# Kernel optimization log

Hardware: AMD Instinct MI355X
Metric: run time of the kernel (lower is better)

Reference implementation:

```python
import jax, jax.numpy as jnp
import numpy as np

N_FILTERS = 40
FILTER_SIZE = 401   # int(16000*25/1000), forced odd
POOL_STRIDE = 160   # int(16000*10/1000)
EPS = 1e-6
S_SMOOTH = 0.04     # fixed PCEN smoothing coefficient s
DELTA = 2.0         # fixed PCEN bias delta
R_MIN, R_MAX = 0.2, 1.0
HIDDEN = 32


def setup_inputs() -> dict:
    key = jax.random.key(0)
    ks = jax.random.split(key, 6)
    B, L = 8, 160000
    x = jax.random.normal(ks[0], (B, L), dtype=jnp.float32)
    # mel-initialized Gabor params (as in mel_filter_params)
    sr, fmin, fmax = 16000.0, 60.0, 7800.0
    min_mel = 1127.0 * np.log1p(fmin / 700.0)
    max_mel = 1127.0 * np.log1p(fmax / 700.0)
    peaks_mel = np.linspace(min_mel, max_mel, N_FILTERS + 2)
    peaks_hz = 700.0 * np.expm1(peaks_mel / 1127.0)
    center_freqs = jnp.asarray(peaks_hz[1:-1] * 2.0 * np.pi / sr, dtype=jnp.float32)
    z = np.sqrt(2.0 * np.log(2.0)) / np.pi
    bandwidths = jnp.asarray(z * sr / (peaks_hz[2:] - peaks_hz[:-2]), dtype=jnp.float32)
    pooling_widths = jnp.full((N_FILTERS,), 0.4, dtype=jnp.float32)
    # GRU (input_size=1, hidden=32) + head Linear(32,32)->ReLU->Linear(32,2)
    def gl(k, shape):
        return jax.random.normal(k, shape, dtype=jnp.float32) * 0.1
    w_ih = gl(ks[1], (3 * HIDDEN, 1))
    w_hh = gl(ks[2], (3 * HIDDEN, HIDDEN))
    b_ih = jnp.zeros((3 * HIDDEN,), jnp.float32)
    b_hh = jnp.zeros((3 * HIDDEN,), jnp.float32)
    hw1 = gl(ks[3], (32, HIDDEN)); hb1 = jnp.zeros((32,), jnp.float32)
    hw2 = gl(ks[4], (2, 32)); hb2 = jnp.zeros((2,), jnp.float32)
    return dict(x=x, center_freqs=center_freqs, bandwidths=bandwidths,
                pooling_widths=pooling_widths, w_ih=w_ih, w_hh=w_hh,
                b_ih=b_ih, b_hh=b_hh, hw1=hw1, hb1=hb1, hw2=hw2, hb2=hb2)


def _gabor_filterbank(x, center_freqs, bandwidths, pooling_widths):
    z = np.sqrt(2.0 * np.log(2.0)) / np.pi
    cf = jnp.clip(center_freqs, 0.0, np.pi)
    bw = jnp.clip(bandwidths, 4.0 * z, FILTER_SIZE * z)
    t = jnp.arange(-(FILTER_SIZE // 2), (FILTER_SIZE + 1) // 2, dtype=jnp.float32)
    denom = 1.0 / (jnp.sqrt(2.0 * np.pi) * bw)                        # [F]
    gauss = jnp.exp(-(t[None, :] ** 2) / (2.0 * bw[:, None] ** 2))    # [F,K]
    phase = cf[:, None] * t[None, :]                                  # [F,K]
    fr = denom[:, None] * gauss * jnp.cos(phase)
    fi = denom[:, None] * gauss * jnp.sin(phase)
    filt = jnp.concatenate([fr, fi], axis=0)[:, None, :]              # [2F,1,K]
    pad = FILTER_SIZE // 2
    y = jax.lax.conv_general_dilated(x[:, None, :], filt, (1,), [(pad, pad)])
    y = y ** 2
    y = y[:, :N_FILTERS] + y[:, N_FILTERS:]                           # squared modulus [B,F,L]
    pw = jnp.clip(pooling_widths, 2.0 / FILTER_SIZE, 0.5)
    tt = jnp.arange(FILTER_SIZE, dtype=jnp.float32) / (FILTER_SIZE - 1) - 0.5
    win = jnp.exp(-0.5 * (tt[None, :] / pw[:, None]) ** 2)[:, None, :]  # [F,1,K]
    y = jax.lax.conv_general_dilated(y, win, (POOL_STRIDE,), [(pad, pad)],
                                     feature_group_count=N_FILTERS)
    return y  # [B,F,T]


def _gru_cell(h, xin, w_ih, w_hh, b_ih, b_hh):
    gi = xin @ w_ih.T + b_ih   # [N,3H]
    gh = h @ w_hh.T + b_hh
    i_r, i_z, i_n = jnp.split(gi, 3, axis=-1)
    h_r, h_z, h_n = jnp.split(gh, 3, axis=-1)
    r = jax.nn.sigmoid(i_r + h_r)
    zz = jax.nn.sigmoid(i_z + h_z)
    n = jnp.tanh(i_n + r * h_n)
    return (1.0 - zz) * n + zz * h


def _adaptive_pcen(frames, w_ih, w_hh, b_ih, b_hh, hw1, hb1, hw2, hb2):
    B, F, T = frames.shape
    Xt = jnp.transpose(frames, (2, 0, 1))  # [T,B,F]

    def controller(x_prev, x_t):  # each [B,F] -> per-bin (alpha, r)
        xp = x_prev.reshape(-1, 1)
        xc = x_t.reshape(-1, 1)
        h = jnp.zeros((B * F, HIDDEN), frames.dtype)
        h = _gru_cell(h, xp, w_ih, w_hh, b_ih, b_hh)
        h = _gru_cell(h, xc, w_ih, w_hh, b_ih, b_hh)
        hid = jax.nn.relu(h @ hw1.T + hb1)
        logits = hid @ hw2.T + hb2  # [B*F,2]
        alpha = jax.nn.sigmoid(logits[:, 0]).reshape(B, F)
        r = (R_MIN + (R_MAX - R_MIN) * jax.nn.sigmoid(logits[:, 1])).reshape(B, F)
        return alpha, r

    def step(carry, X_t):
        M_prev, X_prev = carry
        alpha, r = controller(X_prev, X_t)
        M_t = (1.0 - S_SMOOTH) * M_prev + S_SMOOTH * X_t
        out = (X_t / (M_t + EPS) ** alpha + DELTA) ** r - DELTA ** r
        return (M_t, X_t), out

    init = (jnp.zeros((B, F), frames.dtype), Xt[0])
    _, outs = jax.lax.scan(step, init, Xt)
    return jnp.transpose(outs, (1, 2, 0))  # [B,F,T]


def reference(x, center_freqs, bandwidths, pooling_widths,
              w_ih, w_hh, b_ih, b_hh, hw1, hb1, hw2, hb2):
    frames = _gabor_filterbank(x, center_freqs, bandwidths, pooling_widths)
    return _adaptive_pcen(frames, w_ih, w_hh, b_ih, b_hh, hw1, hb1, hw2, hb2)
```

## Files before the change

### kernel.cpp

```cpp
#include <hip/hip_runtime.h>
#include <math.h>

#define NF 40
#define FS 401
#define AST 424
#define PSTRIDE 160
#define BB 8
#define LL 160000
#define PADL 256
#define LST 161024
#define TOUT 1000
#define NTILE 512
#define NCHUNKC 313
#define ROWCH 121
#define ROWST (ROWCH*8)
#define EROW 522
#define WLEN 416
#define NCONVB 5032

typedef __attribute__((ext_vector_type(8))) _Float16 half8v;
typedef __attribute__((ext_vector_type(4))) _Float16 half4v;
typedef __attribute__((ext_vector_type(2))) _Float16 half2v;
typedef __attribute__((ext_vector_type(4))) float float4v;
typedef _Float16 f16;

__device__ __forceinline__ float sigm(float x) { return 1.0f / (1.0f + __expf(-x)); }
__device__ __forceinline__ float tanh_fast(float x) { return 1.0f - 2.0f / (__expf(2.0f * x) + 1.0f); }

__global__ __launch_bounds__(256) void prep_all(
    const float* __restrict__ x, const float* __restrict__ cf_,
    const float* __restrict__ bw_, const float* __restrict__ pw_,
    f16* __restrict__ xb, f16* __restrict__ Ag, float* __restrict__ Wg)
{
    int blk = blockIdx.x;
    if (blk < NCONVB) {
        int i = blk * 256 + threadIdx.x;
        int b = i / LST, o = i % LST;
        float v = 0.0f;
        if (o >= PADL && o < PADL + LL) v = x[b * LL + (o - PADL)];
        xb[i] = (f16)v;
        return;
    }
    if (blk < NCONVB + 80) {
        const float PI_F = 3.14159265358979323846f;
        int row = blk - NCONVB;
        int f = row >> 1, comp = row & 1;
        float Z = sqrtf(2.0f * logf(2.0f)) / PI_F;
        float cf = fminf(fmaxf(cf_[f], 0.0f), PI_F);
        float bw = fminf(fmaxf(bw_[f], 4.0f * Z), 401.0f * Z);
        float denom = 1.0f / (sqrtf(2.0f * PI_F) * bw);
        float inv2 = 1.0f / (2.0f * bw * bw);
        for (int k = threadIdx.x; k < AST; k += 256) {
            float v = 0.0f;
            if (k < FS) {
                float t = (float)(k - 200);
                float g = denom * expf(-(t * t) * inv2);
                float sv, cv;
                sincosf(cf * t, &sv, &cv);
                v = comp ? g * sv : g * cv;
            }
            Ag[row * AST + k] = (f16)v;
        }
        return;
    }
    int f = blk - (NCONVB + 80);
    float pw = fminf(fmaxf(pw_[f], 2.0f / 401.0f), 0.5f);
    float invpw = 1.0f / pw;
    for (int k = threadIdx.x; k < WLEN; k += 256) {
        float w = 0.0f;
        if (k < FS) {
            float ttv = (float)k * (1.0f / 400.0f) - 0.5f;
            float u = ttv * invpw;
            w = expf(-0.5f * u * u);
        }
        Wg[f * WLEN + k] = w;
    }
}

__global__ __launch_bounds__(256, 2) void conv_pool(
    const f16* __restrict__ xb,
    const f16* __restrict__ Ag,
    const float* __restrict__ Wg,
    float* __restrict__ Pp)
{
    __shared__ __align__(16) unsigned char smem[40 * EROW * 2];
    f16* slab = (f16*)smem;
    f16* eL   = (f16*)smem;

    int chunk = blockIdx.x;
    int bi = blockIdx.y;
    int p0 = chunk * NTILE;
    int pbase = PADL + p0 - 200;
    const f16* xs = xb + (size_t)bi * LST;
    int tid = threadIdx.x;

    for (int sc = tid; sc < 8 * 120; sc += 256) {
        int r = sc / 120, m = sc - r * 120;
        int s0 = pbase + 8 * m + (r & ~1);
        const uint* gp = (const uint*)(xs + s0);
        uint v0 = gp[0], v1 = gp[1], v2 = gp[2], v3 = gp[3], v4 = gp[4];
        if (r & 1) {
            v0 = __builtin_amdgcn_alignbyte(v1, v0, 2);
            v1 = __builtin_amdgcn_alignbyte(v2, v1, 2);
            v2 = __builtin_amdgcn_alignbyte(v3, v2, 2);
            v3 = __builtin_amdgcn_alignbyte(v4, v3, 2);
        }
        *(uint4*)(&slab[r * ROWST + 8 * m]) = make_uint4(v0, v1, v2, v3);
    }
    __syncthreads();

    int wv = tid >> 6, lane = tid & 63, q = lane >> 4, l15 = lane & 15;

    float4v acc[5][8];
#pragma unroll
    for (int t = 0; t < 5; ++t)
#pragma unroll
        for (int s = 0; s < 8; ++s)
            acc[t][s] = (float4v){0.f, 0.f, 0.f, 0.f};

    const f16* aP[5];
    const f16* bPtr[10];
#pragma unroll
    for (int t = 0; t < 5; ++t) aP[t] = Ag + (16 * t + l15) * AST + 8 * q;
#pragma unroll
    for (int s = 0; s < 10; ++s) {
        int pos = 128 * wv + 16 * s + l15;
        bPtr[s] = slab + (pos & 7) * ROWST + 8 * ((pos >> 3) + q);
    }

    half8v bf[8];
#pragma unroll
    for (int s = 0; s < 8; ++s) bf[s] = *(const half8v*)(bPtr[s]);

#pragma unroll
    for (int kk = 0; kk < 13; ++kk) {
        int k = 32 * kk;
        half8v af[5];
#pragma unroll
        for (int t = 0; t < 5; ++t) af[t] = *(const half8v*)(aP[t] + k);
        half8v nb0, nb1;
        if (kk < 12) {
            nb0 = *(const half8v*)(bPtr[8] + k);
            nb1 = *(const half8v*)(bPtr[9] + k);
        }
#pragma unroll
        for (int t = 0; t < 5; ++t)
#pragma unroll
            for (int s = 0; s < 8; ++s)
                acc[t][s] = __builtin_amdgcn_mfma_f32_16x16x32_f16(af[t], bf[s], acc[t][s], 0, 0, 0);
        if (kk < 12) {
#pragma unroll
            for (int s = 0; s < 6; ++s) bf[s] = bf[s + 2];
            bf[6] = nb0; bf[7] = nb1;
        }
    }

    __syncthreads();

#pragma unroll
    for (int t = 0; t < 5; ++t) {
        int f0 = 8 * t + 2 * q;
#pragma unroll
        for (int s = 0; s < 8; ++s) {
            float4v a = acc[t][s];
            int pl = 128 * wv + 16 * s + l15;
            bool ok = (p0 + pl) < LL;
            eL[f0 * EROW + pl] = ok ? (f16)(a.x * a.x + a.y * a.y) : (f16)0.f;
            eL[(f0 + 1) * EROW + pl] = ok ? (f16)(a.z * a.z + a.w * a.w) : (f16)0.f;
        }
    }
    for (int i = tid; i < 40 * 10; i += 256) {
        int r = i / 10, cc = 512 + (i - r * 10);
        eL[r * EROW + cc] = (f16)0.f;
    }
    __syncthreads();

    int tau_lo = (p0 - 41) / 160;
    if (tau_lo < 0) tau_lo = 0;
    int tau_hi = (p0 + 711) / 160;
    if (tau_hi > TOUT - 1) tau_hi = TOUT - 1;
    int npr = (tau_hi - tau_lo + 1) * 40;
    int slot = chunk & 1;

    if (tid < npr) {
        int ta = tid / 40;
        int f = tid - ta * 40;
        int tau = tau_lo + ta;
        int base = tau * 160 - 200 - p0;
        int kstart = base < 0 ? -base : 0;
        int kend = 512 - base; if (kend > 401) kend = 401;
        const f16* ep = eL + f * EROW + base + kstart;
        const float* wp = Wg + f * WLEN + kstart;
        float pa = 0.0f;
#pragma unroll 4
        for (int k = kstart; k < kend; k += 2) {
            half2v e2 = *(const half2v*)ep;
            float2 w2 = *(const float2*)wp;
            pa = fmaf((float)e2[0], w2.x, pa);
            pa = fmaf((float)e2[1], w2.y, pa);
            ep += 2; wp += 2;
        }
        Pp[(((size_t)bi * NF + f) * TOUT + tau) * 2 + slot] = pa;
    }
}

__global__ __launch_bounds__(256) void pcen_scan_kernel(
    const float* __restrict__ Pp, float* __restrict__ X, float* __restrict__ M)
{
    int wid = (blockIdx.x * 256 + threadIdx.x) >> 6;
    int lane = threadIdx.x & 63;
    if (wid >= BB * NF) return;
    const float a1 = 0.96f;
    const float a2 = a1 * a1;
    const float a4 = a2 * a2;
    const float a8 = a4 * a4;
    const float a16 = a8 * a8;
    const float a32 = a16 * a16;
    const float ss = 0.04f;
    float al1 = powf(a1, (float)(lane + 1));
    float carry = 0.0f;
    const float* prow = Pp + (size_t)wid * TOUT * 2;
    float* xrow = X + (size_t)wid * TOUT;
    float* mrow = M + (size_t)wid * TOUT;

    for (int c = 0; c < TOUT; c += 64) {
        int t = c + lane;
        float v = 0.0f;
        if (t < TOUT) {
            int s = t * 160 - 200;
            int cl = (s > 0) ? (s >> 9) : 0;
            int ch = (s + 400) >> 9;
            if (ch > NCHUNKC - 1) ch = NCHUNKC - 1;
            v = prow[2 * t + (cl & 1)];
            if (ch > cl) v += prow[2 * t + ((cl & 1) ^ 1)];
            xrow[t] = v;
        }
        float y = ss * v;
        float u;
        u = __shfl_up(y, 1, 64);  if (lane >= 1)  y = fmaf(a1, u, y);
        u = __shfl_up(y, 2, 64);  if (lane >= 2)  y = fmaf(a2, u, y);
        u = __shfl_up(y, 4, 64);  if (lane >= 4)  y = fmaf(a4, u, y);
        u = __shfl_up(y, 8, 64);  if (lane >= 8)  y = fmaf(a8, u, y);
        u = __shfl_up(y, 16, 64); if (lane >= 16) y = fmaf(a16, u, y);
        u = __shfl_up(y, 32, 64); if (lane >= 32) y = fmaf(a32, u, y);
        y = fmaf(al1, carry, y);
        carry = __shfl(y, 63, 64);
        if (t < TOUT) mrow[t] = y;
    }
}

__global__ __launch_bounds__(256) void pcen_ctrl_mfma(
    const float* __restrict__ X, const float* __restrict__ M,
    const float* __restrict__ w_ih, const float* __restrict__ w_hh,
    const float* __restrict__ b_ih, const float* __restrict__ b_hh,
    const float* __restrict__ hw1, const float* __restrict__ hb1,
    const float* __restrict__ hw2, const float* __restrict__ hb2,
    float* __restrict__ out)
{
    __shared__ f16 s_whhA[96 * 40];
    __shared__ f16 s_w1A[32 * 40];
    __shared__ __align__(16) float4 s_A1[32];
    __shared__ __align__(16) float4 s_A2[32];
    __shared__ float s_hb1[32];
    __shared__ float s_hw2[64];
    __shared__ float s_hb2[2];
    __shared__ f16 sh1[4][16 * 40];
    __shared__ f16 sh2[4][16 * 40];
    __shared__ float sxc[4][16], sxp[4][16], smv[4][16];

    int tid = threadIdx.x;
    for (int i = tid; i < 96 * 32; i += 256) {
        int m = i >> 5, k = i & 31;
        s_whhA[m * 40 + k] = (f16)w_hh[i];
    }
    for (int i = tid; i < 32 * 32; i += 256) {
        int m = i >> 5, k = i & 31;
        s_w1A[m * 40 + k] = (f16)hw1[i];
    }
    if (tid < 32) {
        int j = tid;
        s_A1[j] = make_float4(w_ih[j], b_ih[j] + b_hh[j],
                              w_ih[32 + j], b_ih[32 + j] + b_hh[32 + j]);
        s_A2[j] = make_float4(w_ih[64 + j], b_ih[64 + j], b_hh[64 + j], 0.0f);
        s_hb1[j] = hb1[j];
    }
    if (tid < 64) s_hw2[tid] = hw2[tid];
    if (tid < 2)  s_hb2[tid] = hb2[tid];
    __syncthreads();

    int wv = tid >> 6, lane = tid & 63;
    int c = lane & 15, q = lane >> 4;
    int instBase = blockIdx.x * 64 + wv * 16;

    if (lane < 16) {
        int idx = instBase + lane;
        int t = idx % TOUT;
        float xcv = X[idx];
        float xpv = (t == 0) ? xcv : X[idx - 1];
        sxc[wv][lane] = xcv;
        sxp[wv][lane] = xpv;
        smv[wv][lane] = M[idx];
    }
    float xp = sxp[wv][c];
    float xc = sxc[wv][c];
    float mv = smv[wv][c];

    float h1v[8];
#pragma unroll
    for (int jj = 0; jj < 8; ++jj) {
        int j = (jj < 4) ? (4 * q + jj) : (16 + 4 * q + (jj - 4));
        float4 a1 = s_A1[j];
        float4 a2 = s_A2[j];
        float r = sigm(fmaf(xp, a1.x, a1.y));
        float z = sigm(fmaf(xp, a1.z, a1.w));
        float n = tanh_fast(fmaf(xp, a2.x, a2.y) + r * a2.z);
        h1v[jj] = (1.0f - z) * n;
    }

    {
        half4v lo = {(f16)h1v[0], (f16)h1v[1], (f16)h1v[2], (f16)h1v[3]};
        half4v hi = {(f16)h1v[4], (f16)h1v[5], (f16)h1v[6], (f16)h1v[7]};
        *(half4v*)(&sh1[wv][c * 40 + 4 * q]) = lo;
        *(half4v*)(&sh1[wv][c * 40 + 16 + 4 * q]) = hi;
    }

    float4v acc[6];
    {
        half8v bf = *(const half8v*)(&sh1[wv][c * 40 + 8 * q]);
#pragma unroll
        for (int t = 0; t < 6; ++t) {
            half8v af = *(const half8v*)(&s_whhA[(16 * t + c) * 40 + 8 * q]);
            acc[t] = __builtin_amdgcn_mfma_f32_16x16x32_f16(af, bf, (float4v){0.f,0.f,0.f,0.f}, 0, 0, 0);
        }
    }

    float h2v[8];
#pragma unroll
    for (int jj = 0; jj < 8; ++jj) {
        int j = (jj < 4) ? (4 * q + jj) : (16 + 4 * q + (jj - 4));
        int reg = jj & 3;
        float accR = (jj < 4) ? acc[0][reg] : acc[1][reg];
        float accZ = (jj < 4) ? acc[2][reg] : acc[3][reg];
        float accN = (jj < 4) ? acc[4][reg] : acc[5][reg];
        float4 a1 = s_A1[j];
        float4 a2 = s_A2[j];
        float r = sigm(fmaf(xc, a1.x, a1.y) + accR);
        float z = sigm(fmaf(xc, a1.z, a1.w) + accZ);
        float gn = accN + a2.z;
        float n = tanh_fast(fmaf(xc, a2.x, a2.y) + r * gn);
        h2v[jj] = fmaf(z, h1v[jj] - n, n);
    }

    {
        half4v lo = {(f16)h2v[0], (f16)h2v[1], (f16)h2v[2], (f16)h2v[3]};
        half4v hi = {(f16)h2v[4], (f16)h2v[5], (f16)h2v[6], (f16)h2v[7]};
        *(half4v*)(&sh2[wv][c * 40 + 4 * q]) = lo;
        *(half4v*)(&sh2[wv][c * 40 + 16 + 4 * q]) = hi;
    }

    float4v hacc[2];
    {
        half8v bf = *(const half8v*)(&sh2[wv][c * 40 + 8 * q]);
#pragma unroll
        for (int t = 0; t < 2; ++t) {
            half8v af = *(const half8v*)(&s_w1A[(16 * t + c) * 40 + 8 * q]);
            hacc[t] = __builtin_amdgcn_mfma_f32_16x16x32_f16(af, bf, (float4v){0.f,0.f,0.f,0.f}, 0, 0, 0);
        }
    }

    float p0 = 0.f, p1 = 0.f;
#pragma unroll
    for (int jj = 0; jj < 8; ++jj) {
        int i = (jj < 4) ? (4 * q + jj) : (16 + 4 * q + (jj - 4));
        int reg = jj & 3;
        float hv = (jj < 4) ? hacc[0][reg] : hacc[1][reg];
        hv = fmaxf(hv + s_hb1[i], 0.0f);
        p0 = fmaf(hv, s_hw2[i], p0);
        p1 = fmaf(hv, s_hw2[32 + i], p1);
    }
    p0 += __shfl_xor(p0, 16);
    p0 += __shfl_xor(p0, 32);
    p1 += __shfl_xor(p1, 16);
    p1 += __shfl_xor(p1, 32);

    float alpha = sigm(p0 + s_hb2[0]);
    float rr = fmaf(0.8f, sigm(p1 + s_hb2[1]), 0.2f);
    float md = __expf(alpha * __logf(mv + 1e-6f));
    float bse = xc / md + 2.0f;
    float val = __expf(rr * __logf(bse)) - __expf(rr * 0.69314718056f);
    if (lane < 16)
        out[instBase + lane] = val;
}

extern "C" void kernel_launch(void* const* d_in, const int* in_sizes, int n_in,
                              void* d_out, int out_size, void* d_ws, size_t ws_size,
                              hipStream_t stream) {
    const float* x    = (const float*)d_in[0];
    const float* cf   = (const float*)d_in[1];
    const float* bw   = (const float*)d_in[2];
    const float* pw   = (const float*)d_in[3];
    const float* w_ih = (const float*)d_in[4];
    const float* w_hh = (const float*)d_in[5];
    const float* b_ih = (const float*)d_in[6];
    const float* b_hh = (const float*)d_in[7];
    const float* hw1  = (const float*)d_in[8];
    const float* hb1  = (const float*)d_in[9];
    const float* hw2  = (const float*)d_in[10];
    const float* hb2  = (const float*)d_in[11];
    float* out = (float*)d_out;

    f16* xb   = (f16*)d_ws;
    f16* Ag   = xb + (size_t)BB * LST;
    float* Wg = (float*)(Ag + (size_t)80 * AST);
    float* Pp = Wg + (size_t)NF * WLEN;
    float* Xf = Pp + (size_t)BB * NF * TOUT * 2;
    float* Mf = Xf + (size_t)BB * NF * TOUT;

    prep_all<<<dim3(NCONVB + 80 + 40), dim3(256), 0, stream>>>(
        x, cf, bw, pw, xb, Ag, Wg);

    conv_pool<<<dim3(NCHUNKC, BB), dim3(256), 0, stream>>>(xb, Ag, Wg, Pp);

    pcen_scan_kernel<<<dim3((BB * NF * 64) / 256), dim3(256), 0, stream>>>(Pp, Xf, Mf);
    pcen_ctrl_mfma<<<dim3((BB * NF * TOUT) / 64), dim3(256), 0, stream>>>(
        Xf, Mf, w_ih, w_hh, b_ih, b_hh, hw1, hb1, hw2, hb2, out);
}
```

Before: 296.0 us.

## Parallelize pooling dot products across 16-lane groups with fp16 shifted windows

The pooling stage in conv_pool used to give each (tau, filter) pair to one thread running a long serial loop. It now gives each pair to a 16-lane group that does 8-wide fp16 vector loads from four pre-shifted fp16 copies of the pooling window, then combines the partial sums with shuffles. This removes the serial tail and the misaligned fp32 window reads. In support, Pp is transposed to a tau-major layout, the conv_pool occupancy hint rises from 2 to 3 blocks, and the controller kernel handles four 64-instance groups per block. The trade-off is reduced precision from fp16 pooling weights and more shuffle work.

After: 583.1 us. 1.97x slower.

```diff
diff --git a/kernel.cpp b/kernel.cpp
--- a/kernel.cpp
+++ b/kernel.cpp
@@ -14,8 +14,8 @@
 #define NCHUNKC 313
 #define ROWCH 121
 #define ROWST (ROWCH*8)
-#define EROW 522
-#define WLEN 416
+#define EROW 520
+#define WL2 432
 #define NCONVB 5032
 
 typedef __attribute__((ext_vector_type(8))) _Float16 half8v;
@@ -30,7 +30,7 @@
 __global__ __launch_bounds__(256) void prep_all(
     const float* __restrict__ x, const float* __restrict__ cf_,
     const float* __restrict__ bw_, const float* __restrict__ pw_,
-    f16* __restrict__ xb, f16* __restrict__ Ag, float* __restrict__ Wg)
+    f16* __restrict__ xb, f16* __restrict__ Ag, f16* __restrict__ Wg4)
 {
     int blk = blockIdx.x;
     if (blk < NCONVB) {
@@ -66,21 +66,23 @@
     int f = blk - (NCONVB + 80);
     float pw = fminf(fmaxf(pw_[f], 2.0f / 401.0f), 0.5f);
     float invpw = 1.0f / pw;
-    for (int k = threadIdx.x; k < WLEN; k += 256) {
+    for (int idx = threadIdx.x; idx < 4 * WL2; idx += 256) {
+        int r = idx / WL2, p = idx - r * WL2;
+        int k = p - 2 * r;
         float w = 0.0f;
-        if (k < FS) {
+        if (k >= 0 && k < FS) {
             float ttv = (float)k * (1.0f / 400.0f) - 0.5f;
             float u = ttv * invpw;
             w = expf(-0.5f * u * u);
         }
-        Wg[f * WLEN + k] = w;
+        Wg4[(f * 4 + r) * WL2 + p] = (f16)w;
     }
 }
 
-__global__ __launch_bounds__(256, 2) void conv_pool(
+__global__ __launch_bounds__(256, 3) void conv_pool(
     const f16* __restrict__ xb,
     const f16* __restrict__ Ag,
-    const float* __restrict__ Wg,
+    const f16* __restrict__ Wg4,
     float* __restrict__ Pp)
 {
     __shared__ __align__(16) unsigned char smem[40 * EROW * 2];
@@ -169,8 +171,8 @@
             eL[(f0 + 1) * EROW + pl] = ok ? (f16)(a.z * a.z + a.w * a.w) : (f16)0.f;
         }
     }
-    for (int i = tid; i < 40 * 10; i += 256) {
-        int r = i / 10, cc = 512 + (i - r * 10);
+    for (int i = tid; i < 40 * 8; i += 256) {
+        int r = i >> 3, cc = 512 + (i & 7);
         eL[r * EROW + cc] = (f16)0.f;
     }
     __syncthreads();
@@ -181,26 +183,42 @@
     if (tau_hi > TOUT - 1) tau_hi = TOUT - 1;
     int npr = (tau_hi - tau_lo + 1) * 40;
     int slot = chunk & 1;
-
-    if (tid < npr) {
-        int ta = tid / 40;
-        int f = tid - ta * 40;
+    int gid = tid >> 4;
+    int lg = tid & 15;
+
+    for (int pr = gid; pr < npr; pr += 16) {
+        int ta = pr / 40;
+        int f = pr - ta * 40;
         int tau = tau_lo + ta;
-        int base = tau * 160 - 200 - p0;
-        int kstart = base < 0 ? -base : 0;
-        int kend = 512 - base; if (kend > 401) kend = 401;
-        const f16* ep = eL + f * EROW + base + kstart;
-        const float* wp = Wg + f * WLEN + kstart;
+        int b = tau * 160 - 200 - p0;
+        int bc = b > 0 ? b : 0;
+        int j0 = bc >> 3;
+        int r = (b & 7) >> 1;
+        int pw0 = 8 * j0 - b + 2 * r;
+        int jlast = (b + 400) >> 3;
+        if (jlast > 64) jlast = 64;
+        const f16* ebase = eL + f * EROW;
+        const f16* wbase = Wg4 + ((f * 4 + r) * WL2) + pw0;
         float pa = 0.0f;
-#pragma unroll 4
-        for (int k = kstart; k < kend; k += 2) {
-            half2v e2 = *(const half2v*)ep;
-            float2 w2 = *(const float2*)wp;
-            pa = fmaf((float)e2[0], w2.x, pa);
-            pa = fmaf((float)e2[1], w2.y, pa);
-            ep += 2; wp += 2;
-        }
-        Pp[(((size_t)bi * NF + f) * TOUT + tau) * 2 + slot] = pa;
+#pragma unroll
+        for (int i = 0; i < 4; ++i) {
+            int j = j0 + 16 * i + lg;
+            bool act = (j <= jlast);
+            int jc = act ? j : j0;
+            half8v e8 = *(const half8v*)(ebase + 8 * jc);
+            half8v w8 = *(const half8v*)(wbase + 8 * (jc - j0));
+            if (act) {
+#pragma unroll
+                for (int d = 0; d < 8; ++d)
+                    pa = fmaf((float)e8[d], (float)w8[d], pa);
+            }
+        }
+        pa += __shfl_xor(pa, 1, 16);
+        pa += __shfl_xor(pa, 2, 16);
+        pa += __shfl_xor(pa, 4, 16);
+        pa += __shfl_xor(pa, 8, 16);
+        if (lg == 0)
+            Pp[(((size_t)bi * TOUT + tau) * NF + f) * 2 + slot] = pa;
     }
 }
 
@@ -219,7 +237,8 @@
     const float ss = 0.04f;
     float al1 = powf(a1, (float)(lane + 1));
     float carry = 0.0f;
-    const float* prow = Pp + (size_t)wid * TOUT * 2;
+    int bi = wid / NF, f = wid - bi * NF;
+    const float* pbase = Pp + (size_t)bi * TOUT * NF * 2 + f * 2;
     float* xrow = X + (size_t)wid * TOUT;
     float* mrow = M + (size_t)wid * TOUT;
 
@@ -231,8 +250,8 @@
             int cl = (s > 0) ? (s >> 9) : 0;
             int ch = (s + 400) >> 9;
             if (ch > NCHUNKC - 1) ch = NCHUNKC - 1;
-            v = prow[2 * t + (cl & 1)];
-            if (ch > cl) v += prow[2 * t + ((cl & 1) ^ 1)];
+            v = pbase[(size_t)t * NF * 2 + (cl & 1)];
+            if (ch > cl) v += pbase[(size_t)t * NF * 2 + ((cl & 1) ^ 1)];
             xrow[t] = v;
         }
         float y = ss * v;
@@ -290,106 +309,109 @@
 
     int wv = tid >> 6, lane = tid & 63;
     int c = lane & 15, q = lane >> 4;
-    int instBase = blockIdx.x * 64 + wv * 16;
-
-    if (lane < 16) {
-        int idx = instBase + lane;
-        int t = idx % TOUT;
-        float xcv = X[idx];
-        float xpv = (t == 0) ? xcv : X[idx - 1];
-        sxc[wv][lane] = xcv;
-        sxp[wv][lane] = xpv;
-        smv[wv][lane] = M[idx];
-    }
-    float xp = sxp[wv][c];
-    float xc = sxc[wv][c];
-    float mv = smv[wv][c];
-
-    float h1v[8];
-#pragma unroll
-    for (int jj = 0; jj < 8; ++jj) {
-        int j = (jj < 4) ? (4 * q + jj) : (16 + 4 * q + (jj - 4));
-        float4 a1 = s_A1[j];
-        float4 a2 = s_A2[j];
-        float r = sigm(fmaf(xp, a1.x, a1.y));
-        float z = sigm(fmaf(xp, a1.z, a1.w));
-        float n = tanh_fast(fmaf(xp, a2.x, a2.y) + r * a2.z);
-        h1v[jj] = (1.0f - z) * n;
-    }
-
-    {
-        half4v lo = {(f16)h1v[0], (f16)h1v[1], (f16)h1v[2], (f16)h1v[3]};
-        half4v hi = {(f16)h1v[4], (f16)h1v[5], (f16)h1v[6], (f16)h1v[7]};
-        *(half4v*)(&sh1[wv][c * 40 + 4 * q]) = lo;
-        *(half4v*)(&sh1[wv][c * 40 + 16 + 4 * q]) = hi;
-    }
-
-    float4v acc[6];
-    {
-        half8v bf = *(const half8v*)(&sh1[wv][c * 40 + 8 * q]);
-#pragma unroll
-        for (int t = 0; t < 6; ++t) {
-            half8v af = *(const half8v*)(&s_whhA[(16 * t + c) * 40 + 8 * q]);
-            acc[t] = __builtin_amdgcn_mfma_f32_16x16x32_f16(af, bf, (float4v){0.f,0.f,0.f,0.f}, 0, 0, 0);
-        }
-    }
-
-    float h2v[8];
-#pragma unroll
-    for (int jj = 0; jj < 8; ++jj) {
-        int j = (jj < 4) ? (4 * q + jj) : (16 + 4 * q + (jj - 4));
-        int reg = jj & 3;
-        float accR = (jj < 4) ? acc[0][reg] : acc[1][reg];
-        float accZ = (jj < 4) ? acc[2][reg] : acc[3][reg];
-        float accN = (jj < 4) ? acc[4][reg] : acc[5][reg];
-        float4 a1 = s_A1[j];
-        float4 a2 = s_A2[j];
-        float r = sigm(fmaf(xc, a1.x, a1.y) + accR);
-        float z = sigm(fmaf(xc, a1.z, a1.w) + accZ);
-        float gn = accN + a2.z;
-        float n = tanh_fast(fmaf(xc, a2.x, a2.y) + r * gn);
-        h2v[jj] = fmaf(z, h1v[jj] - n, n);
-    }
-
-    {
-        half4v lo = {(f16)h2v[0], (f16)h2v[1], (f16)h2v[2], (f16)h2v[3]};
-        half4v hi = {(f16)h2v[4], (f16)h2v[5], (f16)h2v[6], (f16)h2v[7]};
-        *(half4v*)(&sh2[wv][c * 40 + 4 * q]) = lo;
-        *(half4v*)(&sh2[wv][c * 40 + 16 + 4 * q]) = hi;
-    }
-
-    float4v hacc[2];
-    {
-        half8v bf = *(const half8v*)(&sh2[wv][c * 40 + 8 * q]);
-#pragma unroll
-        for (int t = 0; t < 2; ++t) {
-            half8v af = *(const half8v*)(&s_w1A[(16 * t + c) * 40 + 8 * q]);
-            hacc[t] = __builtin_amdgcn_mfma_f32_16x16x32_f16(af, bf, (float4v){0.f,0.f,0.f,0.f}, 0, 0, 0);
-        }
-    }
-
-    float p0 = 0.f, p1 = 0.f;
-#pragma unroll
-    for (int jj = 0; jj < 8; ++jj) {
-        int i = (jj < 4) ? (4 * q + jj) : (16 + 4 * q + (jj - 4));
-        int reg = jj & 3;
-        float hv = (jj < 4) ? hacc[0][reg] : hacc[1][reg];
-        hv = fmaxf(hv + s_hb1[i], 0.0f);
-        p0 = fmaf(hv, s_hw2[i], p0);
-        p1 = fmaf(hv, s_hw2[32 + i], p1);
-    }
-    p0 += __shfl_xor(p0, 16);
-    p0 += __shfl_xor(p0, 32);
-    p1 += __shfl_xor(p1, 16);
-    p1 += __shfl_xor(p1, 32);
-
-    float alpha = sigm(p0 + s_hb2[0]);
-    float rr = fmaf(0.8f, sigm(p1 + s_hb2[1]), 0.2f);
-    float md = __expf(alpha * __logf(mv + 1e-6f));
-    float bse = xc / md + 2.0f;
-    float val = __expf(rr * __logf(bse)) - __expf(rr * 0.69314718056f);
-    if (lane < 16)
-        out[instBase + lane] = val;
+
+    for (int rep = 0; rep < 4; ++rep) {
+        int instBase = blockIdx.x * 256 + rep * 64 + wv * 16;
+
+        if (lane < 16) {
+            int idx = instBase + lane;
+            int t = idx % TOUT;
+            float xcv = X[idx];
+            float xpv = (t == 0) ? xcv : X[idx - 1];
+            sxc[wv][lane] = xcv;
+            sxp[wv][lane] = xpv;
+            smv[wv][lane] = M[idx];
+        }
+        float xp = sxp[wv][c];
+        float xc = sxc[wv][c];
+        float mv = smv[wv][c];
+
+        float h1v[8];
+#pragma unroll
+        for (int jj = 0; jj < 8; ++jj) {
+            int j = (jj < 4) ? (4 * q + jj) : (16 + 4 * q + (jj - 4));
+            float4 a1 = s_A1[j];
+            float4 a2 = s_A2[j];
+            float r = sigm(fmaf(xp, a1.x, a1.y));
+            float z = sigm(fmaf(xp, a1.z, a1.w));
+            float n = tanh_fast(fmaf(xp, a2.x, a2.y) + r * a2.z);
+            h1v[jj] = (1.0f - z) * n;
+        }
+
+        {
+            half4v lo = {(f16)h1v[0], (f16)h1v[1], (f16)h1v[2], (f16)h1v[3]};
+            half4v hi = {(f16)h1v[4], (f16)h1v[5], (f16)h1v[6], (f16)h1v[7]};
+            *(half4v*)(&sh1[wv][c * 40 + 4 * q]) = lo;
+            *(half4v*)(&sh1[wv][c * 40 + 16 + 4 * q]) = hi;
+        }
+
+        float4v acc[6];
+        {
+            half8v bf = *(const half8v*)(&sh1[wv][c * 40 + 8 * q]);
+#pragma unroll
+            for (int t = 0; t < 6; ++t) {
+                half8v af = *(const half8v*)(&s_whhA[(16 * t + c) * 40 + 8 * q]);
+                acc[t] = __builtin_amdgcn_mfma_f32_16x16x32_f16(af, bf, (float4v){0.f,0.f,0.f,0.f}, 0, 0, 0);
+            }
+        }
+
+        float h2v[8];
+#pragma unroll
+        for (int jj = 0; jj < 8; ++jj) {
+            int j = (jj < 4) ? (4 * q + jj) : (16 + 4 * q + (jj - 4));
+            int reg = jj & 3;
+            float accR = (jj < 4) ? acc[0][reg] : acc[1][reg];
+            float accZ = (jj < 4) ? acc[2][reg] : acc[3][reg];
+            float accN = (jj < 4) ? acc[4][reg] : acc[5][reg];
+            float4 a1 = s_A1[j];
+            float4 a2 = s_A2[j];
+            float r = sigm(fmaf(xc, a1.x, a1.y) + accR);
+            float z = sigm(fmaf(xc, a1.z, a1.w) + accZ);
+            float gn = accN + a2.z;
+            float n = tanh_fast(fmaf(xc, a2.x, a2.y) + r * gn);
+            h2v[jj] = fmaf(z, h1v[jj] - n, n);
+        }
+
+        {
+            half4v lo = {(f16)h2v[0], (f16)h2v[1], (f16)h2v[2], (f16)h2v[3]};
+            half4v hi = {(f16)h2v[4], (f16)h2v[5], (f16)h2v[6], (f16)h2v[7]};
+            *(half4v*)(&sh2[wv][c * 40 + 4 * q]) = lo;
+            *(half4v*)(&sh2[wv][c * 40 + 16 + 4 * q]) = hi;
+        }
+
+        float4v hacc[2];
+        {
+            half8v bf = *(const half8v*)(&sh2[wv][c * 40 + 8 * q]);
+#pragma unroll
+            for (int t = 0; t < 2; ++t) {
+                half8v af = *(const half8v*)(&s_w1A[(16 * t + c) * 40 + 8 * q]);
+                hacc[t] = __builtin_amdgcn_mfma_f32_16x16x32_f16(af, bf, (float4v){0.f,0.f,0.f,0.f}, 0, 0, 0);
+            }
+        }
+
+        float p0 = 0.f, p1 = 0.f;
+#pragma unroll
+        for (int jj = 0; jj < 8; ++jj) {
+            int i = (jj < 4) ? (4 * q + jj) : (16 + 4 * q + (jj - 4));
+            int reg = jj & 3;
+            float hv = (jj < 4) ? hacc[0][reg] : hacc[1][reg];
+            hv = fmaxf(hv + s_hb1[i], 0.0f);
+            p0 = fmaf(hv, s_hw2[i], p0);
+            p1 = fmaf(hv, s_hw2[32 + i], p1);
+        }
+        p0 += __shfl_xor(p0, 16);
+        p0 += __shfl_xor(p0, 32);
+        p1 += __shfl_xor(p1, 16);
+        p1 += __shfl_xor(p1, 32);
+
+        float alpha = sigm(p0 + s_hb2[0]);
+        float rr = fmaf(0.8f, sigm(p1 + s_hb2[1]), 0.2f);
+        float md = __expf(alpha * __logf(mv + 1e-6f));
+        float bse = xc / md + 2.0f;
+        float val = __expf(rr * __logf(bse)) - __expf(rr * 0.69314718056f);
+        if (lane < 16)
+            out[instBase + lane] = val;
+    }
 }
 
 extern "C" void kernel_launch(void* const* d_in, const int* in_sizes, int n_in,
@@ -411,17 +433,17 @@
 
     f16* xb   = (f16*)d_ws;
     f16* Ag   = xb + (size_t)BB * LST;
-    float* Wg = (float*)(Ag + (size_t)80 * AST);
-    float* Pp = Wg + (size_t)NF * WLEN;
-    float* Xf = Pp + (size_t)BB * NF * TOUT * 2;
+    f16* Wg4  = Ag + (size_t)80 * AST;
+    float* Pp = (float*)(Wg4 + (size_t)NF * 4 * WL2);
+    float* Xf = Pp + (size_t)BB * TOUT * NF * 2;
     float* Mf = Xf + (size_t)BB * NF * TOUT;
 
     prep_all<<<dim3(NCONVB + 80 + 40), dim3(256), 0, stream>>>(
-        x, cf, bw, pw, xb, Ag, Wg);
-
-    conv_pool<<<dim3(NCHUNKC, BB), dim3(256), 0, stream>>>(xb, Ag, Wg, Pp);
+        x, cf, bw, pw, xb, Ag, Wg4);
+
+    conv_pool<<<dim3(NCHUNKC, BB), dim3(256), 0, stream>>>(xb, Ag, Wg4, Pp);
 
     pcen_scan_kernel<<<dim3((BB * NF * 64) / 256), dim3(256), 0, stream>>>(Pp, Xf, Mf);
-    pcen_ctrl_mfma<<<dim3((BB * NF * TOUT) / 64), dim3(256), 0, stream>>>(
+    pcen_ctrl_mfma<<<dim3((BB * NF * TOUT) / 256), dim3(256), 0, stream>>>(
         Xf, Mf, w_ih, w_hh, b_ih, b_hh, hw1, hb1, hw2, hb2, out);
 }
```
